# Performance work log

Measured on AMD Instinct MI355X. Metric: run time of the kernel, lower is better.

Reference implementation:

```python
import jax, jax.numpy as jnp
import numpy as np
from jax import lax

_DN = ('NCHW', 'OIHW', 'NCHW')


def _depthwise_kernel(C):
    base = jnp.array([[0.1, 0.1, 0.1], [0.1, 0.2, 0.1], [0.1, 0.1, 0.1]], jnp.float32)
    return jnp.broadcast_to(base[None, None], (C, 1, 3, 3))


def setup_inputs() -> dict:
    key = jax.random.key(0)
    k0, k1, k2 = jax.random.split(key, 3)
    T, B, C, H, W = 16, 16, 8, 128, 128
    hidden = max(1, C // 16)  # reduction_ratio = 16
    events = jax.random.normal(k0, (T, B, C, H, W), jnp.float32)
    conv_w = _depthwise_kernel(C)  # fixed neighbor kernel from _initialize_weights
    att_w1 = jax.random.normal(k1, (hidden, 2 * C), jnp.float32) / np.sqrt(2 * C)
    att_w2 = jax.random.normal(k2, (C, hidden), jnp.float32) / np.sqrt(hidden)
    return {
        'events': events,
        'conv_w': conv_w,
        'att_w1': att_w1,
        'att_w2': att_w2,
        'density_w': jnp.array(1.0, jnp.float32),
        'temporal_w': jnp.array(0.8, jnp.float32),
        'motion_w': jnp.array(0.5, jnp.float32),
    }


def _forward(events, conv_w, att_w1, att_w2, density_w, temporal_w, motion_w):
    T, B, C, H, W = events.shape
    x = events.reshape(T * B, C, H, W)
    # depthwise 3x3 neighbor conv (groups=C), batched over all T steps at once
    wi = lax.conv_general_dilated(x, conv_w, (1, 1), 'SAME',
                                  dimension_numbers=_DN, feature_group_count=C)
    # --- BALIFBetaAdaptor: max/avg pool -> 1x1 convs (== matmuls) -> sigmoid ---
    mx = jnp.max(x, axis=(2, 3))            # (TB, C)
    av = jnp.mean(x, axis=(2, 3))           # (TB, C)
    pooled = jnp.concatenate([mx, av], axis=1)  # (TB, 2C)
    h = jax.nn.relu(pooled @ att_w1.T)
    beta = (0.5 + 0.45 * jax.nn.sigmoid(h @ att_w2.T)).reshape(T, B, C, 1, 1)
    # --- LightweightEventAdaptor: density / temporal change / unfold variance ---
    density = jnp.mean(x, axis=(1, 2, 3)).reshape(T, B)
    diff = jnp.mean(jnp.abs(events[1:] - events[:-1]), axis=(2, 3, 4))
    temporal = jnp.concatenate([jnp.zeros((1, B), events.dtype), diff], axis=0)  # t=0 -> 0
    # F.unfold(k=3,pad=1) variance over dim=1 (C*9 values, unbiased) via sum-convs
    ones_k = jnp.ones((1, C, 3, 3), events.dtype)
    s1 = lax.conv_general_dilated(x, ones_k, (1, 1), 'SAME', dimension_numbers=_DN)
    s2 = lax.conv_general_dilated(x * x, ones_k, (1, 1), 'SAME', dimension_numbers=_DN)
    n = C * 9
    var = (s2 - s1 * s1 / n) / (n - 1)      # (TB,1,H,W), matches torch.var (ddof=1)
    motion = jnp.mean(var, axis=(1, 2, 3)).reshape(T, B)
    adj = jax.nn.sigmoid(density_w * density + temporal_w * temporal + motion_w * motion) * 2.0
    thr = (1.0 + adj).reshape(T, B, 1, 1, 1)  # base_threshold = 1.0
    wi = wi.reshape(T, B, C, H, W)

    # --- sequential LIF charge/fire/reset (torch.no_grad -> stop_gradient) ---
    def step(v, inp):
        w, b, th, cur = inp
        v = lax.stop_gradient(b * v + (1.0 - b) * w)              # charge
        spike = lax.stop_gradient(jnp.arctan(2.0 * (v - th)) * 0.5 + 0.5)  # atan surrogate
        v = lax.stop_gradient((1.0 - spike) * v)                  # reset (v_reset = 0)
        return v, cur * spike

    v0 = jnp.zeros((B, C, H, W), events.dtype)
    _, out = lax.scan(step, v0, (wi, beta, thr, events))
    return out  # (T,B,C,H,W)


def reference(events, conv_w, att_w1, att_w2, density_w, temporal_w, motion_w):
    return _forward(events, conv_w, att_w1, att_w2, density_w, temporal_w, motion_w)
```

## Files before the change

### kernel.cpp

```cpp
#include <hip/hip_runtime.h>
#include <math.h>

#define T_ 16
#define B_ 16
#define C_ 8
#define H_ 128
#define W_ 128
#define HW_ (H_*W_)
#define CHW_ (C_*HW_)
#define NSL 16
#define NV 19

__device__ __forceinline__ float wave_sum(float v){
    #pragma unroll
    for (int o=32;o>0;o>>=1) v += __shfl_down(v,o,64);
    return v;
}
__device__ __forceinline__ float wave_max(float v){
    #pragma unroll
    for (int o=32;o>0;o>>=1) v = fmaxf(v,__shfl_down(v,o,64));
    return v;
}

__global__ __launch_bounds__(256, 4) void stats_stream_kernel(
    const float* __restrict__ events, float* __restrict__ partials,
    float* __restrict__ yfield)
{
    int bid = blockIdx.x;
    int s   = bid & 15;
    int tb  = bid >> 4;
    int t   = tb >> 4;
    int tid = threadIdx.x;
    int r   = tid >> 5;
    int c0  = (tid & 31) * 4;
    int gh  = s*8 + r;

    const float* frame = events + (size_t)tb*CHW_ + gh*W_ + c0;
    const float* prev  = frame - (size_t)B_*CHW_;

    float4 xv[C_];
    #pragma unroll
    for (int c=0;c<C_;c++) xv[c] = *reinterpret_cast<const float4*>(frame + c*HW_);

    float dsum = 0.f;
    if (t > 0){
        #pragma unroll
        for (int c=0;c<C_;c++){
            float4 p = *reinterpret_cast<const float4*>(prev + c*HW_);
            float4 x = xv[c];
            dsum += fabsf(x.x-p.x)+fabsf(x.y-p.y)
                  + fabsf(x.z-p.z)+fabsf(x.w-p.w);
        }
    }

    float sumc[C_], maxc[C_];
    float4 y; y.x=0.f; y.y=0.f; y.z=0.f; y.w=0.f;
    float q0=0.f,q1=0.f,q2=0.f,q3=0.f;
    #pragma unroll
    for (int c=0;c<C_;c++){
        float4 x = xv[c];
        y.x+=x.x; y.y+=x.y; y.z+=x.z; y.w+=x.w;
        q0=fmaf(x.x,x.x,q0); q1=fmaf(x.y,x.y,q1);
        q2=fmaf(x.z,x.z,q2); q3=fmaf(x.w,x.w,q3);
        sumc[c] = (x.x+x.y)+(x.z+x.w);
        maxc[c] = fmaxf(fmaxf(x.x,x.y),fmaxf(x.z,x.w));
    }
    float cnt0 = (c0==0)      ? 2.f : 3.f;
    float cnt3 = (c0+3==W_-1) ? 2.f : 3.f;
    float cnth = (gh==0 || gh==H_-1) ? 2.f : 3.f;
    float m2 = cnth * (q0*cnt0 + (q1+q2)*3.f + q3*cnt3);

    *reinterpret_cast<float4*>(yfield + (size_t)tb*HW_ + gh*W_ + c0) = y;

    float vals[NV];
    #pragma unroll
    for (int c=0;c<C_;c++){ vals[c]=sumc[c]; vals[8+c]=maxc[c]; }
    vals[16]=dsum; vals[17]=0.f; vals[18]=m2;

    __shared__ float red[4][NV];
    int lane = tid & 63, wv = tid >> 6;
    #pragma unroll
    for (int i=0;i<NV;i++){
        float rr = (i>=8 && i<16) ? wave_max(vals[i]) : wave_sum(vals[i]);
        if (lane==0) red[wv][i] = rr;
    }
    __syncthreads();
    if (tid < NV){
        float a = red[0][tid], b2 = red[1][tid], c = red[2][tid], d = red[3][tid];
        float rr = (tid>=8 && tid<16) ? fmaxf(fmaxf(a,b2),fmaxf(c,d)) : ((a+b2)+(c+d));
        partials[((size_t)tb*NSL + s)*NV + tid] = rr;
    }
}

__global__ __launch_bounds__(256) void m1_kernel(
    const float* __restrict__ yfield, float* __restrict__ m1p)
{
    int bid = blockIdx.x;
    int s   = bid & 7;
    int tb  = bid >> 3;
    int h0  = s*16;
    int tid = threadIdx.x;
    __shared__ float yb[18][W_];

    const float* yf = yfield + (size_t)tb*HW_;
    for (int i = tid; i < 18*32; i += 256){
        int rr = i >> 5, cc = (i & 31) * 4;
        int gh = h0 - 1 + rr;
        float4 v; v.x=0.f; v.y=0.f; v.z=0.f; v.w=0.f;
        if (gh >= 0 && gh < H_) v = *reinterpret_cast<const float4*>(yf + gh*W_ + cc);
        *reinterpret_cast<float4*>(&yb[rr][cc]) = v;
    }
    __syncthreads();

    float m1 = 0.f;
    {
        int w  = tid & 127;
        int rg = tid >> 7;
        bool hasL = (w>0), hasR = (w<W_-1);
        int base = rg*8;
        const float* row;
        row = yb[base];   float a0 = row[w] + (hasL?row[w-1]:0.f) + (hasR?row[w+1]:0.f);
        row = yb[base+1]; float a1 = row[w] + (hasL?row[w-1]:0.f) + (hasR?row[w+1]:0.f);
        #pragma unroll
        for (int i=0;i<8;i++){
            row = yb[base+2+i];
            float a2 = row[w] + (hasL?row[w-1]:0.f) + (hasR?row[w+1]:0.f);
            float s1 = a0 + a1 + a2;
            m1 = fmaf(s1, s1, m1);
            a0 = a1; a1 = a2;
        }
    }
    m1 = wave_sum(m1);
    __shared__ float red2[4];
    int lane = tid & 63, wv = tid >> 6;
    if (lane==0) red2[wv] = m1;
    __syncthreads();
    if (tid==0) m1p[bid] = (red2[0]+red2[1])+(red2[2]+red2[3]);
}

__global__ __launch_bounds__(64) void combine_kernel(
    const float* __restrict__ partials,
    const float* __restrict__ m1p,
    const float* __restrict__ att_w1,
    const float* __restrict__ att_w2,
    const float* __restrict__ dwp, const float* __restrict__ twp,
    const float* __restrict__ mwp,
    float* __restrict__ beta_out, float* __restrict__ thr_out,
    float* __restrict__ zeropad)
{
    int tb = blockIdx.x;
    int t  = tb / B_;
    int i  = threadIdx.x;
    if (tb == 0 && i < 16) zeropad[i] = 0.f;
    __shared__ float v[NV];
    if (i < NV){
        if (i == 17){
            const float* mp = m1p + (size_t)tb*8;
            float acc = 0.f;
            #pragma unroll
            for (int k=0;k<8;k++) acc += mp[k];
            v[17] = acc;
        } else {
            const float* p = partials + (size_t)tb*NSL*NV;
            bool mx = (i>=8 && i<16);
            float acc = p[i];
            #pragma unroll
            for (int k=1;k<NSL;k++){
                float x = p[k*NV + i];
                acc = mx ? fmaxf(acc, x) : (acc + x);
            }
            v[i] = acc;
        }
    }
    __syncthreads();
    if (i == 0){
        float h1 = 0.f;
        for (int c=0;c<C_;c++) h1 += v[8+c] * att_w1[c];
        for (int c=0;c<C_;c++) h1 += (v[c]/(float)HW_) * att_w1[C_+c];
        h1 = fmaxf(h1, 0.f);
        float total = 0.f;
        for (int c=0;c<C_;c++) total += v[c];
        float density  = total / (float)CHW_;
        float temporal = (t==0) ? 0.f : v[16] / (float)CHW_;
        float motion   = (v[18] - v[17]/72.f) / 71.f / (float)HW_;
        float z = dwp[0]*density + twp[0]*temporal + mwp[0]*motion;
        float adj = 2.f / (1.f + expf(-z));
        thr_out[tb] = 1.f + adj;
        for (int c=0;c<C_;c++){
            float sg = 1.f / (1.f + expf(-(h1 * att_w2[c])));
            beta_out[tb*C_ + c] = 0.5f + 0.45f*sg;
        }
    }
}

__device__ __forceinline__ void gload16(const float* src, float* lds_dst){
    __builtin_amdgcn_global_load_lds(
        (const __attribute__((address_space(1))) unsigned int*)src,
        (__attribute__((address_space(3))) unsigned int*)lds_dst, 16, 0, 0);
}

__device__ __forceinline__ float fast_atan(float x){
    float ax = fabsf(x);
    bool inv = ax > 1.f;
    float z  = inv ? __builtin_amdgcn_rcpf(ax) : ax;
    float z2 = z*z;
    float p = -0.0117212f;
    p = fmaf(p, z2,  0.05265332f);
    p = fmaf(p, z2, -0.11643287f);
    p = fmaf(p, z2,  0.19354346f);
    p = fmaf(p, z2, -0.33262347f);
    p = fmaf(p, z2,  0.99997726f);
    p = p * z;
    float r = inv ? (1.57079632679f - p) : p;
    return copysignf(r, x);
}

#define SROWS 10

__global__ __launch_bounds__(256, 8) void lif_kernel(
    const float* __restrict__ events,
    const float* __restrict__ conv_w,
    const float* __restrict__ beta,
    const float* __restrict__ thr,
    const float* __restrict__ zeropad,
    float* __restrict__ out)
{
    int bid  = blockIdx.x;
    int hblk = bid & 15;
    int bc   = bid >> 4;
    int b = bc >> 3, c = bc & 7;
    int h0 = hblk * 8;
    int tid = threadIdx.x;
    int wv  = tid >> 6;

    float wk[9];
    #pragma unroll
    for (int k=0;k<9;k++) wk[k] = conv_w[c*9 + k];

    __shared__ float lds[2][SROWS*W_];

    int idxA = tid,        rowA = idxA >> 5, colA = (idxA & 31) * 4;
    int idxB = 256 + tid,  rowB = idxB >> 5, colB = (idxB & 31) * 4;
    int ghA = h0 - 1 + rowA;
    int ghB = h0 - 1 + rowB;
    bool okA = (ghA >= 0) && (ghA < H_);
    bool okB = (ghB >= 0) && (ghB < H_);
    const float* baseFrame = events + ((size_t)(b * C_) + c) * HW_;
    const float* srcA0 = okA ? (baseFrame + ghA*W_ + colA) : zeropad;
    const float* srcB0 = okB ? (baseFrame + ghB*W_ + colB) : zeropad;
    const size_t tstep = (size_t)B_ * CHW_;
    size_t stepA = okA ? tstep : 0;
    size_t stepB = okB ? tstep : 0;

    int w  = tid & 127;
    int rg = tid >> 7;
    int rbase = rg * 4;
    int wl = (w > 0)    ? w-1 : 0;
    int wr = (w < W_-1) ? w+1 : W_-1;
    bool hasL = (w > 0), hasR = (w < W_-1);

    float v[4];
    #pragma unroll
    for (int i=0;i<4;i++) v[i] = 0.f;

    gload16(srcA0, &lds[0][wv*256]);
    if (wv == 0) gload16(srcB0, &lds[0][1024]);

    const float* bp = beta + (b*C_ + c);
    const float* tp = thr + b;
    float bv = bp[0];
    float th = tp[0];

    for (int t = 0; t < T_; ++t){
        int cur = t & 1, nxt = cur ^ 1;
        __syncthreads();

        if (t + 1 < T_){
            gload16(srcA0 + (size_t)(t+1)*stepA, &lds[nxt][wv*256]);
            if (wv == 0) gload16(srcB0 + (size_t)(t+1)*stepB, &lds[nxt][1024]);
        }
        float bvn = (t+1 < T_) ? bp[(size_t)(t+1)*B_*C_] : 0.f;
        float thn = (t+1 < T_) ? tp[(size_t)(t+1)*B_]    : 0.f;

        const float* L = &lds[cur][0];
        float omb = 1.f - bv;
        float* op = out + ((size_t)(t*B_+b)*C_ + c)*HW_ + h0*W_;

        const float* row0 = L + rbase*W_;
        const float* row1 = row0 + W_;
        float la = hasL ? row0[wl] : 0.f;  float ma = row0[w];  float ra = hasR ? row0[wr] : 0.f;
        float lb = hasL ? row1[wl] : 0.f;  float mb = row1[w];  float rb = hasR ? row1[wr] : 0.f;

        #pragma unroll
        for (int i=0;i<4;i++){
            const float* rowc = L + (rbase+2+i)*W_;
            float lc = hasL ? rowc[wl] : 0.f;
            float mc = rowc[w];
            float rc = hasR ? rowc[wr] : 0.f;
            float wi = wk[0]*la + wk[1]*ma + wk[2]*ra
                     + wk[3]*lb + wk[4]*mb + wk[5]*rb
                     + wk[6]*lc + wk[7]*mc + wk[8]*rc;
            float vv = fmaf(bv, v[i], omb*wi);
            float sp = fast_atan(2.f*(vv - th))*0.5f + 0.5f;
            op[(rbase+i)*W_ + w] = mb * sp;
            v[i] = (1.f - sp) * vv;
            la=lb; ma=mb; ra=rb; lb=lc; mb=mc; rb=rc;
        }
        __syncthreads();

        bv = bvn; th = thn;
    }
}

extern "C" void kernel_launch(void* const* d_in, const int* in_sizes, int n_in,
                              void* d_out, int out_size, void* d_ws, size_t ws_size,
                              hipStream_t stream)
{
    const float* events = (const float*)d_in[0];
    const float* conv_w = (const float*)d_in[1];
    const float* att_w1 = (const float*)d_in[2];
    const float* att_w2 = (const float*)d_in[3];
    const float* dwp    = (const float*)d_in[4];
    const float* twp    = (const float*)d_in[5];
    const float* mwp    = (const float*)d_in[6];
    float* out = (float*)d_out;

    float* ws       = (float*)d_ws;
    float* partials = ws;
    float* m1p      = partials + (size_t)T_*B_*NSL*NV;
    float* beta     = m1p + (size_t)T_*B_*8;
    float* thr      = beta + (size_t)T_*B_*C_;
    float* zeropad  = thr + T_*B_;
    float* yfield   = zeropad + 16;

    stats_stream_kernel<<<T_*B_*NSL, 256, 0, stream>>>(events, partials, yfield);
    m1_kernel          <<<T_*B_*8,   256, 0, stream>>>(yfield, m1p);
    combine_kernel     <<<T_*B_,     64,  0, stream>>>(partials, m1p, att_w1, att_w2,
                                                       dwp, twp, mwp, beta, thr, zeropad);
    lif_kernel         <<<B_*C_*16,  256, 0, stream>>>(events, conv_w, beta, thr, zeropad, out);
}
```

Measured before the change: 100.3 us.

## Restructure stats kernel to stream time chunks and reuse previous frame in registers

The stats kernel now has each block walk 4 consecutive time steps for one batch and row slice. The previous frame stays in registers, so the temporal-difference term no longer re-reads the prior frame from memory. The channel sum is built through shared memory, and partials are stored per channel with a new layout that the combine kernel reduces. The LIF output store also becomes nontemporal. This cuts the extra read of events for the diff at the cost of fewer blocks, a serial time loop with syncthreads, and a larger partial reduction in combine.

Result: faster. 95.37 us (-4.9%).

```diff
diff --git a/kernel.cpp b/kernel.cpp
--- a/kernel.cpp
+++ b/kernel.cpp
@@ -8,8 +8,8 @@
 #define W_ 128
 #define HW_ (H_*W_)
 #define CHW_ (C_*HW_)
+#define TC 4
 #define NSL 16
-#define NV 19
 
 __device__ __forceinline__ float wave_sum(float v){
     #pragma unroll
@@ -22,73 +22,98 @@
     return v;
 }
 
-__global__ __launch_bounds__(256, 4) void stats_stream_kernel(
+__global__ __launch_bounds__(512, 4) void stats_kernel(
     const float* __restrict__ events, float* __restrict__ partials,
     float* __restrict__ yfield)
 {
-    int bid = blockIdx.x;
-    int s   = bid & 15;
-    int tb  = bid >> 4;
-    int t   = tb >> 4;
-    int tid = threadIdx.x;
-    int r   = tid >> 5;
-    int c0  = (tid & 31) * 4;
-    int gh  = s*8 + r;
-
-    const float* frame = events + (size_t)tb*CHW_ + gh*W_ + c0;
-    const float* prev  = frame - (size_t)B_*CHW_;
-
-    float4 xv[C_];
-    #pragma unroll
-    for (int c=0;c<C_;c++) xv[c] = *reinterpret_cast<const float4*>(frame + c*HW_);
-
-    float dsum = 0.f;
-    if (t > 0){
-        #pragma unroll
-        for (int c=0;c<C_;c++){
-            float4 p = *reinterpret_cast<const float4*>(prev + c*HW_);
-            float4 x = xv[c];
-            dsum += fabsf(x.x-p.x)+fabsf(x.y-p.y)
-                  + fabsf(x.z-p.z)+fabsf(x.w-p.w);
-        }
-    }
-
-    float sumc[C_], maxc[C_];
-    float4 y; y.x=0.f; y.y=0.f; y.z=0.f; y.w=0.f;
-    float q0=0.f,q1=0.f,q2=0.f,q3=0.f;
-    #pragma unroll
-    for (int c=0;c<C_;c++){
-        float4 x = xv[c];
-        y.x+=x.x; y.y+=x.y; y.z+=x.z; y.w+=x.w;
-        q0=fmaf(x.x,x.x,q0); q1=fmaf(x.y,x.y,q1);
-        q2=fmaf(x.z,x.z,q2); q3=fmaf(x.w,x.w,q3);
-        sumc[c] = (x.x+x.y)+(x.z+x.w);
-        maxc[c] = fmaxf(fmaxf(x.x,x.y),fmaxf(x.z,x.w));
-    }
-    float cnt0 = (c0==0)      ? 2.f : 3.f;
-    float cnt3 = (c0+3==W_-1) ? 2.f : 3.f;
+    int bid   = blockIdx.x;
+    int chunk = bid & 3;
+    int s     = (bid >> 2) & 15;
+    int b     = bid >> 6;
+    int t0    = chunk * TC;
+    int gh0   = s * 8;
+    int tid   = threadIdx.x;
+    int c     = tid >> 6;
+    int lane  = tid & 63;
+
+    __shared__ float xs[C_][1024];
+
+    int lrow  = lane >> 3;
+    int lcol0 = (lane & 7) * 16;
+    int gh    = gh0 + lrow;
     float cnth = (gh==0 || gh==H_-1) ? 2.f : 3.f;
-    float m2 = cnth * (q0*cnt0 + (q1+q2)*3.f + q3*cnt3);
-
-    *reinterpret_cast<float4*>(yfield + (size_t)tb*HW_ + gh*W_ + c0) = y;
-
-    float vals[NV];
-    #pragma unroll
-    for (int c=0;c<C_;c++){ vals[c]=sumc[c]; vals[8+c]=maxc[c]; }
-    vals[16]=dsum; vals[17]=0.f; vals[18]=m2;
-
-    __shared__ float red[4][NV];
-    int lane = tid & 63, wv = tid >> 6;
-    #pragma unroll
-    for (int i=0;i<NV;i++){
-        float rr = (i>=8 && i<16) ? wave_max(vals[i]) : wave_sum(vals[i]);
-        if (lane==0) red[wv][i] = rr;
-    }
-    __syncthreads();
-    if (tid < NV){
-        float a = red[0][tid], b2 = red[1][tid], c = red[2][tid], d = red[3][tid];
-        float rr = (tid>=8 && tid<16) ? fmaxf(fmaxf(a,b2),fmaxf(c,d)) : ((a+b2)+(c+d));
-        partials[((size_t)tb*NSL + s)*NV + tid] = rr;
+    float w0  = (lcol0==0)        ? 2.f : 3.f;
+    float w15 = (lcol0+15==W_-1)  ? 2.f : 3.f;
+
+    const float* base0 = events + (size_t)(t0*B_+b)*CHW_ + c*HW_ + gh*W_ + lcol0;
+    const size_t tstep = (size_t)B_ * CHW_;
+
+    float px[16];
+    if (t0 > 0){
+        const float* pp = base0 - tstep;
+        #pragma unroll
+        for (int e=0;e<16;e+=4){
+            float4 v = *reinterpret_cast<const float4*>(pp + e);
+            px[e]=v.x; px[e+1]=v.y; px[e+2]=v.z; px[e+3]=v.w;
+        }
+    } else {
+        #pragma unroll
+        for (int e=0;e<16;e++) px[e]=0.f;
+    }
+
+    #pragma unroll 1
+    for (int tt=0; tt<TC; ++tt){
+        int t = t0 + tt;
+        const float* src = base0 + (size_t)tt*tstep;
+
+        float cx[16];
+        #pragma unroll
+        for (int e=0;e<16;e+=4){
+            float4 v = *reinterpret_cast<const float4*>(src + e);
+            cx[e]=v.x; cx[e+1]=v.y; cx[e+2]=v.z; cx[e+3]=v.w;
+        }
+
+        float ssum=0.f, smax=-INFINITY, q=0.f, dsu=0.f;
+        #pragma unroll
+        for (int e=0;e<16;e++){
+            float x = cx[e];
+            ssum += x;
+            smax = fmaxf(smax, x);
+            float w = (e==0) ? w0 : ((e==15) ? w15 : 3.f);
+            q = fmaf(w*x, x, q);
+            dsu += fabsf(x - px[e]);
+            px[e] = x;
+        }
+
+        #pragma unroll
+        for (int e=0;e<16;e+=4){
+            float4 v; v.x=cx[e]; v.y=cx[e+1]; v.z=cx[e+2]; v.w=cx[e+3];
+            *reinterpret_cast<float4*>(&xs[c][lane*16 + e]) = v;
+        }
+        __syncthreads();
+
+        {
+            int p0 = tid * 2;
+            float y0=0.f, y1=0.f;
+            #pragma unroll
+            for (int cc=0; cc<C_; cc++){
+                y0 += xs[cc][p0];
+                y1 += xs[cc][p0+1];
+            }
+            float2 yy; yy.x=y0; yy.y=y1;
+            *reinterpret_cast<float2*>(yfield + (size_t)(t*B_+b)*HW_ + gh0*W_ + p0) = yy;
+        }
+
+        float rs = wave_sum(ssum);
+        float rm = wave_max(smax);
+        float rd = wave_sum(dsu);
+        float rq = wave_sum(cnth * q);
+        if (lane == 0){
+            float4 o; o.x=rs; o.y=rm; o.z=rd; o.w=rq;
+            *reinterpret_cast<float4*>(
+                partials + (((size_t)(t*B_+b)*NSL + s)*C_ + c)*4) = o;
+        }
+        __syncthreads();
     }
 }
 
@@ -152,25 +177,33 @@
     int t  = tb / B_;
     int i  = threadIdx.x;
     if (tb == 0 && i < 16) zeropad[i] = 0.f;
-    __shared__ float v[NV];
-    if (i < NV){
-        if (i == 17){
-            const float* mp = m1p + (size_t)tb*8;
-            float acc = 0.f;
-            #pragma unroll
-            for (int k=0;k<8;k++) acc += mp[k];
-            v[17] = acc;
-        } else {
-            const float* p = partials + (size_t)tb*NSL*NV;
-            bool mx = (i>=8 && i<16);
-            float acc = p[i];
-            #pragma unroll
-            for (int k=1;k<NSL;k++){
-                float x = p[k*NV + i];
-                acc = mx ? fmaxf(acc, x) : (acc + x);
-            }
-            v[i] = acc;
-        }
+    __shared__ float v[19];
+    const float* p = partials + (size_t)tb*NSL*C_*4;
+    if (i < 8){
+        float acc = 0.f;
+        #pragma unroll
+        for (int s=0;s<NSL;s++) acc += p[(s*C_ + i)*4 + 0];
+        v[i] = acc;
+    } else if (i < 16){
+        int c = i - 8;
+        float acc = -INFINITY;
+        #pragma unroll
+        for (int s=0;s<NSL;s++) acc = fmaxf(acc, p[(s*C_ + c)*4 + 1]);
+        v[i] = acc;
+    } else if (i == 16){
+        float acc = 0.f;
+        for (int k=0;k<NSL*C_;k++) acc += p[k*4 + 2];
+        v[16] = acc;
+    } else if (i == 17){
+        const float* mp = m1p + (size_t)tb*8;
+        float acc = 0.f;
+        #pragma unroll
+        for (int k=0;k<8;k++) acc += mp[k];
+        v[17] = acc;
+    } else if (i == 18){
+        float acc = 0.f;
+        for (int k=0;k<NSL*C_;k++) acc += p[k*4 + 3];
+        v[18] = acc;
     }
     __syncthreads();
     if (i == 0){
@@ -302,7 +335,7 @@
                      + wk[6]*lc + wk[7]*mc + wk[8]*rc;
             float vv = fmaf(bv, v[i], omb*wi);
             float sp = fast_atan(2.f*(vv - th))*0.5f + 0.5f;
-            op[(rbase+i)*W_ + w] = mb * sp;
+            __builtin_nontemporal_store(mb * sp, &op[(rbase+i)*W_ + w]);
             v[i] = (1.f - sp) * vv;
             la=lb; ma=mb; ra=rb; lb=lc; mb=mc; rb=rc;
         }
@@ -327,15 +360,15 @@
 
     float* ws       = (float*)d_ws;
     float* partials = ws;
-    float* m1p      = partials + (size_t)T_*B_*NSL*NV;
+    float* m1p      = partials + (size_t)T_*B_*NSL*C_*4;
     float* beta     = m1p + (size_t)T_*B_*8;
     float* thr      = beta + (size_t)T_*B_*C_;
     float* zeropad  = thr + T_*B_;
     float* yfield   = zeropad + 16;
 
-    stats_stream_kernel<<<T_*B_*NSL, 256, 0, stream>>>(events, partials, yfield);
-    m1_kernel          <<<T_*B_*8,   256, 0, stream>>>(yfield, m1p);
-    combine_kernel     <<<T_*B_,     64,  0, stream>>>(partials, m1p, att_w1, att_w2,
-                                                       dwp, twp, mwp, beta, thr, zeropad);
-    lif_kernel         <<<B_*C_*16,  256, 0, stream>>>(events, conv_w, beta, thr, zeropad, out);
-}
+    stats_kernel  <<<B_*NSL*4,  512, 0, stream>>>(events, partials, yfield);
+    m1_kernel     <<<T_*B_*8,   256, 0, stream>>>(yfield, m1p);
+    combine_kernel<<<T_*B_,     64,  0, stream>>>(partials, m1p, att_w1, att_w2,
+                                                  dwp, twp, mwp, beta, thr, zeropad);
+    lif_kernel    <<<B_*C_*16,  256, 0, stream>>>(events, conv_w, beta, thr, zeropad, out);
+}
```
